# Optimization experiments

Measured on AMD Instinct MI355X. Metric: run time of the kernel, lower is better.

## Reference

```python
import jax, jax.numpy as jnp
import numpy as np

ALPHA = 1.0

def setup_inputs() -> dict:
    key = jax.random.key(0)
    k1, k2, k3, k4 = jax.random.split(key, 4)
    B, N, D = 2048, 32768, 128
    return {
        "anchor": jax.random.normal(k1, (B, D), dtype=jnp.float32),
        "positive": jax.random.normal(k2, (B, D), dtype=jnp.float32),
        "negative": jax.random.normal(k3, (N, D), dtype=jnp.float32),
        "r_score": jax.random.normal(k4, (B, 1), dtype=jnp.float32),
    }

def reference(anchor, positive, negative, r_score):
    # pos_sim: [B,1] elementwise dot per row
    pos_sim = jnp.sum(anchor * positive, axis=1, keepdims=True)
    # neg_mul: [B,N] score matrix; row-wise stable logsumexp -> [B,1]
    neg_mul = jnp.matmul(anchor, negative.T)
    neg_sim = jax.scipy.special.logsumexp(neg_mul, axis=1, keepdims=True)
    loss = jax.nn.relu(neg_sim - pos_sim + r_score + ALPHA)
    return jnp.mean(loss)
```

## Files before the change

kernel.cpp:

```cpp
#include <hip/hip_runtime.h>
#include <hip/hip_bf16.h>


#define B_ROWS 2048
#define N_NEG  32768
#define DIM    128
#define LOG2E  1.4426950408889634f
#define LN2    0.6931471805599453f

typedef __bf16 bf16x8 __attribute__((ext_vector_type(8)));
typedef float  f32x4  __attribute__((ext_vector_type(4)));

static __device__ inline unsigned short f2bf(float f) {
    union { float f; unsigned u; } v; v.f = f;
    unsigned r = v.u + 0x7FFF + ((v.u >> 16) & 1);
    return (unsigned short)(r >> 16);
}

static __device__ inline void load_lds16(const void* g, void* s) {
    __builtin_amdgcn_global_load_lds(
        (const __attribute__((address_space(1))) void*)g,
        (__attribute__((address_space(3))) void*)s,
        16, 0, 0);
}

__global__ void prep(const float* __restrict__ anchor,
                     const float* __restrict__ positive,
                     const float* __restrict__ neg,
                     unsigned short* __restrict__ a_bf,
                     unsigned short* __restrict__ n_bf,
                     float* __restrict__ pos_sim,
                     float* __restrict__ sumexp) {
    int t = threadIdx.x;
    if (blockIdx.x < 256) {
        int row = blockIdx.x * 8 + (t >> 5);
        int c4  = (t & 31) * 4;
        const float4 a4 = *(const float4*)(anchor   + row * DIM + c4);
        const float4 p4 = *(const float4*)(positive + row * DIM + c4);
        float dot = a4.x * p4.x + a4.y * p4.y + a4.z * p4.z + a4.w * p4.w;
        ushort4 ab;
        ab.x = f2bf(a4.x * LOG2E); ab.y = f2bf(a4.y * LOG2E);
        ab.z = f2bf(a4.z * LOG2E); ab.w = f2bf(a4.w * LOG2E);
        *(ushort4*)(a_bf + row * DIM + c4) = ab;
        #pragma unroll
        for (int m = 1; m <= 16; m <<= 1) dot += __shfl_xor(dot, m, 64);
        if ((t & 31) == 0) { pos_sim[row] = dot; sumexp[row] = 0.0f; }
    } else {
        int i = (blockIdx.x - 256) * 256 + t;
        #pragma unroll
        for (int k = 0; k < 4; k++) {
            int idx = i + k * (1024 * 256);
            float4 v = *(const float4*)(neg + (size_t)idx * 4);
            ushort4 o;
            o.x = f2bf(v.x); o.y = f2bf(v.y); o.z = f2bf(v.z); o.w = f2bf(v.w);
            *(ushort4*)(n_bf + (size_t)idx * 4) = o;
        }
    }
}

#define CHUNK 1024
#define TSTEPS (CHUNK / 128)

__global__ __launch_bounds__(256, 2) void fused_gemm_lse(
        const unsigned short* __restrict__ A,
        const unsigned short* __restrict__ Nb,
        float* __restrict__ sumexp) {
    __shared__ unsigned short lds[2][128 * 128];

    const int bid     = blockIdx.x;
    const int rowTile = bid & 15;
    const int chunk   = bid >> 4;
    const int wave = threadIdx.x >> 6, lane = threadIdx.x & 63;
    const int wr = wave >> 1, wc = wave & 1;
    const int q = lane >> 4, c = lane & 15;
    const int lrow = lane >> 4;
    const int lchk = lane & 15;

    const unsigned short* Ag = A + rowTile * (128 * DIM);
    const unsigned short* Bg = Nb + (size_t)(chunk * CHUNK) * DIM;

    #pragma unroll
    for (int i = 0; i < 8; i++) {
        int off = wave * 4096 + i * 512;
        int r   = (off >> 7) + lrow;
        int gofs = r * DIM + ((lchk ^ (r & 7)) << 3);
        load_lds16(Ag + gofs, &lds[0][off]);
        load_lds16(Bg + gofs, &lds[1][off]);
    }
    asm volatile("s_waitcnt vmcnt(0)" ::: "memory");
    __syncthreads();

    int swz[4];
    #pragma unroll
    for (int k = 0; k < 4; k++) swz[k] = (((k * 4 + q) ^ (c & 7)) << 3);

    bf16x8 af[4][4];
    #pragma unroll
    for (int i = 0; i < 4; i++) {
        int row = wr * 64 + i * 16 + c;
        #pragma unroll
        for (int k = 0; k < 4; k++)
            af[i][k] = *(const bf16x8*)&lds[0][row * DIM + swz[k]];
    }
    __syncthreads();

    const f32x4 zero4 = {0.f, 0.f, 0.f, 0.f};
    f32x4 sumacc[4] = {zero4, zero4, zero4, zero4};

    for (int t = 0; t < TSTEPS; t++) {
        const int cur = 1 - (t & 1);
        const int nxt = t & 1;
        if (t + 1 < TSTEPS) {
            const unsigned short* Bn = Bg + (size_t)(t + 1) * 128 * DIM;
            #pragma unroll
            for (int i = 0; i < 8; i++) {
                int off = wave * 4096 + i * 512;
                int r   = (off >> 7) + lrow;
                int gofs = r * DIM + ((lchk ^ (r & 7)) << 3);
                load_lds16(Bn + gofs, &lds[nxt][off]);
            }
        }
        #pragma unroll
        for (int j = 0; j < 4; j++) {
            int brow = wc * 64 + j * 16 + c;
            bf16x8 bf[4];
            #pragma unroll
            for (int k = 0; k < 4; k++)
                bf[k] = *(const bf16x8*)&lds[cur][brow * DIM + swz[k]];
            #pragma unroll
            for (int i = 0; i < 4; i++) {
                f32x4 acc = __builtin_amdgcn_mfma_f32_16x16x32_bf16(af[i][0], bf[0], zero4, 0, 0, 0);
                acc = __builtin_amdgcn_mfma_f32_16x16x32_bf16(af[i][1], bf[1], acc, 0, 0, 0);
                acc = __builtin_amdgcn_mfma_f32_16x16x32_bf16(af[i][2], bf[2], acc, 0, 0, 0);
                acc = __builtin_amdgcn_mfma_f32_16x16x32_bf16(af[i][3], bf[3], acc, 0, 0, 0);
                sumacc[i][0] += __builtin_amdgcn_exp2f(acc[0]);
                sumacc[i][1] += __builtin_amdgcn_exp2f(acc[1]);
                sumacc[i][2] += __builtin_amdgcn_exp2f(acc[2]);
                sumacc[i][3] += __builtin_amdgcn_exp2f(acc[3]);
            }
        }
        if (t + 1 < TSTEPS) {
            asm volatile("s_waitcnt vmcnt(0)" ::: "memory");
            __syncthreads();
        }
    }

    #pragma unroll
    for (int i = 0; i < 4; i++) {
        #pragma unroll
        for (int r = 0; r < 4; r++) {
            float v = sumacc[i][r];
            v += __shfl_xor(v, 1, 64);
            v += __shfl_xor(v, 2, 64);
            v += __shfl_xor(v, 4, 64);
            v += __shfl_xor(v, 8, 64);
            if ((lane & 15) == 0) {
                int row = rowTile * 128 + wr * 64 + i * 16 + q * 4 + r;
                atomicAdd(&sumexp[row], v);
            }
        }
    }
}

__global__ void finalize(const float* __restrict__ sumexp,
                         const float* __restrict__ pos_sim,
                         const float* __restrict__ r_score,
                         float* __restrict__ out) {
    __shared__ float red[4];
    int t = threadIdx.x;
    float acc = 0.0f;
    #pragma unroll
    for (int i = 0; i < 8; i++) {
        int row = t + i * 256;
        float lse  = __log2f(sumexp[row]) * LN2;
        float loss = lse - pos_sim[row] + r_score[row] + 1.0f;
        acc += fmaxf(loss, 0.0f);
    }
    #pragma unroll
    for (int m = 1; m <= 32; m <<= 1) acc += __shfl_xor(acc, m, 64);
    if ((t & 63) == 0) red[t >> 6] = acc;
    __syncthreads();
    if (t == 0) out[0] = (red[0] + red[1] + red[2] + red[3]) * (1.0f / (float)B_ROWS);
}

extern "C" void kernel_launch(void* const* d_in, const int* in_sizes, int n_in,
                              void* d_out, int out_size, void* d_ws, size_t ws_size,
                              hipStream_t stream) {
    const float* anchor   = (const float*)d_in[0];
    const float* positive = (const float*)d_in[1];
    const float* negative = (const float*)d_in[2];
    const float* r_score  = (const float*)d_in[3];
    float* out = (float*)d_out;

    char* ws = (char*)d_ws;
    float* sumexp           = (float*)ws;
    float* pos_sim          = (float*)(ws + 8192);
    unsigned short* a_bf    = (unsigned short*)(ws + 16384);
    unsigned short* n_bf    = (unsigned short*)(ws + 16384 + 524288);

    prep<<<1280, 256, 0, stream>>>(anchor, positive, negative, a_bf, n_bf, pos_sim, sumexp);
    fused_gemm_lse<<<512, 256, 0, stream>>>(a_bf, n_bf, sumexp);
    finalize<<<1, 256, 0, stream>>>(sumexp, pos_sim, r_score, out);
}
```

Before: 95.44 us.

## Keep negatives tile in registers, stream anchors, fuse finalize via last-block counter

The GEMM+logsumexp kernel is restructured so each 512-thread block owns 128 negative rows, holds them in registers as MFMA B operands, and streams all 2048 anchor rows through double-buffered LDS. Each wave loads and reads only its own anchor rows, so the per-step block barrier is gone. Partial sums are staged in LDS and then atomically added per row. The separate finalize kernel is folded in through a completion counter, with the last block computing the mean. The grid drops to 256 blocks and the global atomics per block grow to 2048, which raises contention on the 2048 sumexp addresses.

```diff
diff --git a/kernel.cpp b/kernel.cpp
--- a/kernel.cpp
+++ b/kernel.cpp
@@ -7,6 +7,7 @@
 #define DIM    128
 #define LOG2E  1.4426950408889634f
 #define LN2    0.6931471805599453f
+#define NBLK   256
 
 typedef __bf16 bf16x8 __attribute__((ext_vector_type(8)));
 typedef float  f32x4  __attribute__((ext_vector_type(4)));
@@ -30,9 +31,11 @@
                      unsigned short* __restrict__ a_bf,
                      unsigned short* __restrict__ n_bf,
                      float* __restrict__ pos_sim,
-                     float* __restrict__ sumexp) {
+                     float* __restrict__ sumexp,
+                     int* __restrict__ cnt) {
     int t = threadIdx.x;
     if (blockIdx.x < 256) {
+        if (blockIdx.x == 0 && t == 0) *cnt = 0;
         int row = blockIdx.x * 8 + (t >> 5);
         int c4  = (t & 31) * 4;
         const float4 a4 = *(const float4*)(anchor   + row * DIM + c4);
@@ -58,34 +61,34 @@
     }
 }
 
-#define CHUNK 1024
-#define TSTEPS (CHUNK / 128)
-
-__global__ __launch_bounds__(256, 2) void fused_gemm_lse(
+__global__ __launch_bounds__(512, 2) void fused_gemm_lse(
         const unsigned short* __restrict__ A,
         const unsigned short* __restrict__ Nb,
-        float* __restrict__ sumexp) {
-    __shared__ unsigned short lds[2][128 * 128];
-
-    const int bid     = blockIdx.x;
-    const int rowTile = bid & 15;
-    const int chunk   = bid >> 4;
-    const int wave = threadIdx.x >> 6, lane = threadIdx.x & 63;
-    const int wr = wave >> 1, wc = wave & 1;
+        float* __restrict__ sumexp,
+        const float* __restrict__ pos_sim,
+        const float* __restrict__ r_score,
+        int* __restrict__ cnt,
+        float* __restrict__ out) {
+    __shared__ unsigned short ldsB[128 * 128];
+    __shared__ unsigned short ldsA[2][128 * 128];
+    __shared__ float sumLDS[B_ROWS];
+    __shared__ float red[8];
+    __shared__ int isLast;
+
+    const int tid  = threadIdx.x;
+    const int wave = tid >> 6, lane = tid & 63;
     const int q = lane >> 4, c = lane & 15;
-    const int lrow = lane >> 4;
-    const int lchk = lane & 15;
-
-    const unsigned short* Ag = A + rowTile * (128 * DIM);
-    const unsigned short* Bg = Nb + (size_t)(chunk * CHUNK) * DIM;
-
-    #pragma unroll
-    for (int i = 0; i < 8; i++) {
-        int off = wave * 4096 + i * 512;
+    const int lrow = q, lchk = c;
+    const int bid  = blockIdx.x;
+
+    const unsigned short* Bg = Nb + (size_t)bid * 128 * DIM;
+    #pragma unroll
+    for (int i = 0; i < 4; i++) {
+        int off = wave * 2048 + i * 512;
         int r   = (off >> 7) + lrow;
         int gofs = r * DIM + ((lchk ^ (r & 7)) << 3);
-        load_lds16(Ag + gofs, &lds[0][off]);
-        load_lds16(Bg + gofs, &lds[1][off]);
+        load_lds16(Bg + gofs, &ldsB[off]);
+        load_lds16(A  + gofs, &ldsA[0][off]);
     }
     asm volatile("s_waitcnt vmcnt(0)" ::: "memory");
     __syncthreads();
@@ -94,93 +97,94 @@
     #pragma unroll
     for (int k = 0; k < 4; k++) swz[k] = (((k * 4 + q) ^ (c & 7)) << 3);
 
-    bf16x8 af[4][4];
-    #pragma unroll
-    for (int i = 0; i < 4; i++) {
-        int row = wr * 64 + i * 16 + c;
+    bf16x8 bfr[8][4];
+    #pragma unroll
+    for (int j = 0; j < 8; j++)
         #pragma unroll
         for (int k = 0; k < 4; k++)
-            af[i][k] = *(const bf16x8*)&lds[0][row * DIM + swz[k]];
-    }
-    __syncthreads();
+            bfr[j][k] = *(const bf16x8*)&ldsB[(j * 16 + c) * DIM + swz[k]];
 
     const f32x4 zero4 = {0.f, 0.f, 0.f, 0.f};
-    f32x4 sumacc[4] = {zero4, zero4, zero4, zero4};
-
-    for (int t = 0; t < TSTEPS; t++) {
-        const int cur = 1 - (t & 1);
-        const int nxt = t & 1;
-        if (t + 1 < TSTEPS) {
-            const unsigned short* Bn = Bg + (size_t)(t + 1) * 128 * DIM;
+    const int arow = wave * 16 + c;
+
+    for (int t = 0; t < 16; t++) {
+        const unsigned short* ldsCur = ldsA[t & 1];
+        if (t < 15) {
+            const unsigned short* Ag = A + (size_t)(t + 1) * 128 * DIM;
+            unsigned short* dst = &ldsA[(t + 1) & 1][0];
             #pragma unroll
-            for (int i = 0; i < 8; i++) {
-                int off = wave * 4096 + i * 512;
+            for (int i = 0; i < 4; i++) {
+                int off = wave * 2048 + i * 512;
                 int r   = (off >> 7) + lrow;
                 int gofs = r * DIM + ((lchk ^ (r & 7)) << 3);
-                load_lds16(Bn + gofs, &lds[nxt][off]);
+                load_lds16(Ag + gofs, dst + off);
             }
-        }
-        #pragma unroll
-        for (int j = 0; j < 4; j++) {
-            int brow = wc * 64 + j * 16 + c;
-            bf16x8 bf[4];
-            #pragma unroll
-            for (int k = 0; k < 4; k++)
-                bf[k] = *(const bf16x8*)&lds[cur][brow * DIM + swz[k]];
-            #pragma unroll
-            for (int i = 0; i < 4; i++) {
-                f32x4 acc = __builtin_amdgcn_mfma_f32_16x16x32_bf16(af[i][0], bf[0], zero4, 0, 0, 0);
-                acc = __builtin_amdgcn_mfma_f32_16x16x32_bf16(af[i][1], bf[1], acc, 0, 0, 0);
-                acc = __builtin_amdgcn_mfma_f32_16x16x32_bf16(af[i][2], bf[2], acc, 0, 0, 0);
-                acc = __builtin_amdgcn_mfma_f32_16x16x32_bf16(af[i][3], bf[3], acc, 0, 0, 0);
-                sumacc[i][0] += __builtin_amdgcn_exp2f(acc[0]);
-                sumacc[i][1] += __builtin_amdgcn_exp2f(acc[1]);
-                sumacc[i][2] += __builtin_amdgcn_exp2f(acc[2]);
-                sumacc[i][3] += __builtin_amdgcn_exp2f(acc[3]);
-            }
-        }
-        if (t + 1 < TSTEPS) {
+            asm volatile("s_waitcnt vmcnt(4)" ::: "memory");
+        } else {
             asm volatile("s_waitcnt vmcnt(0)" ::: "memory");
-            __syncthreads();
-        }
-    }
+        }
+
+        bf16x8 af[4];
+        #pragma unroll
+        for (int k = 0; k < 4; k++)
+            af[k] = *(const bf16x8*)&ldsCur[arow * DIM + swz[k]];
+
+        f32x4 sum4 = zero4;
+        #pragma unroll
+        for (int j = 0; j < 8; j++) {
+            f32x4 acc = __builtin_amdgcn_mfma_f32_16x16x32_bf16(af[0], bfr[j][0], zero4, 0, 0, 0);
+            acc = __builtin_amdgcn_mfma_f32_16x16x32_bf16(af[1], bfr[j][1], acc, 0, 0, 0);
+            acc = __builtin_amdgcn_mfma_f32_16x16x32_bf16(af[2], bfr[j][2], acc, 0, 0, 0);
+            acc = __builtin_amdgcn_mfma_f32_16x16x32_bf16(af[3], bfr[j][3], acc, 0, 0, 0);
+            sum4[0] += __builtin_amdgcn_exp2f(acc[0]);
+            sum4[1] += __builtin_amdgcn_exp2f(acc[1]);
+            sum4[2] += __builtin_amdgcn_exp2f(acc[2]);
+            sum4[3] += __builtin_amdgcn_exp2f(acc[3]);
+        }
+        float v0 = sum4[0], v1 = sum4[1], v2 = sum4[2], v3 = sum4[3];
+        #pragma unroll
+        for (int m = 1; m <= 8; m <<= 1) {
+            v0 += __shfl_xor(v0, m, 64);
+            v1 += __shfl_xor(v1, m, 64);
+            v2 += __shfl_xor(v2, m, 64);
+            v3 += __shfl_xor(v3, m, 64);
+        }
+        if ((lane & 15) == 0) {
+            f32x4 w = {v0, v1, v2, v3};
+            *(f32x4*)&sumLDS[t * 128 + wave * 16 + q * 4] = w;
+        }
+    }
+    __syncthreads();
 
     #pragma unroll
     for (int i = 0; i < 4; i++) {
-        #pragma unroll
-        for (int r = 0; r < 4; r++) {
-            float v = sumacc[i][r];
-            v += __shfl_xor(v, 1, 64);
-            v += __shfl_xor(v, 2, 64);
-            v += __shfl_xor(v, 4, 64);
-            v += __shfl_xor(v, 8, 64);
-            if ((lane & 15) == 0) {
-                int row = rowTile * 128 + wr * 64 + i * 16 + q * 4 + r;
-                atomicAdd(&sumexp[row], v);
-            }
-        }
-    }
-}
-
-__global__ void finalize(const float* __restrict__ sumexp,
-                         const float* __restrict__ pos_sim,
-                         const float* __restrict__ r_score,
-                         float* __restrict__ out) {
-    __shared__ float red[4];
-    int t = threadIdx.x;
+        int row = tid + i * 512;
+        atomicAdd(&sumexp[row], sumLDS[row]);
+    }
+    __threadfence();
+    __syncthreads();
+    if (tid == 0) isLast = (atomicAdd(cnt, 1) == NBLK - 1);
+    __syncthreads();
+    if (!isLast) return;
+
     float acc = 0.0f;
     #pragma unroll
-    for (int i = 0; i < 8; i++) {
-        int row = t + i * 256;
-        float lse  = __log2f(sumexp[row]) * LN2;
-        float loss = lse - pos_sim[row] + r_score[row] + 1.0f;
+    for (int i = 0; i < 4; i++) {
+        int row = tid + i * 512;
+        float se   = atomicAdd(&sumexp[row], 0.0f);
+        float loss = __log2f(se) * LN2 - pos_sim[row] + r_score[row] + 1.0f;
         acc += fmaxf(loss, 0.0f);
     }
     #pragma unroll
     for (int m = 1; m <= 32; m <<= 1) acc += __shfl_xor(acc, m, 64);
-    if ((t & 63) == 0) red[t >> 6] = acc;
-    __syncthreads();
-    if (t == 0) out[0] = (red[0] + red[1] + red[2] + red[3]) * (1.0f / (float)B_ROWS);
+    if (lane == 0) red[wave] = acc;
+    __syncthreads();
+    if (tid == 0) {
+        float s = 0.0f;
+        #pragma unroll
+        for (int w = 0; w < 8; w++) s += red[w];
+        out[0] = s * (1.0f / (float)B_ROWS);
+    }
 }
 
 extern "C" void kernel_launch(void* const* d_in, const int* in_sizes, int n_in,
@@ -193,12 +197,14 @@
     float* out = (float*)d_out;
 
     char* ws = (char*)d_ws;
-    float* sumexp           = (float*)ws;
-    float* pos_sim          = (float*)(ws + 8192);
-    unsigned short* a_bf    = (unsigned short*)(ws + 16384);
-    unsigned short* n_bf    = (unsigned short*)(ws + 16384 + 524288);
-
-    prep<<<1280, 256, 0, stream>>>(anchor, positive, negative, a_bf, n_bf, pos_sim, sumexp);
-    fused_gemm_lse<<<512, 256, 0, stream>>>(a_bf, n_bf, sumexp);
-    finalize<<<1, 256, 0, stream>>>(sumexp, pos_sim, r_score, out);
-}
+    float* sumexp        = (float*)ws;
+    float* pos_sim       = (float*)(ws + 8192);
+    int*   cnt           = (int*)(ws + 16384);
+    unsigned short* a_bf = (unsigned short*)(ws + 32768);
+    unsigned short* n_bf = (unsigned short*)(ws + 32768 + 524288);
+
+    prep<<<1280, 256, 0, stream>>>(anchor, positive, negative, a_bf, n_bf,
+                                   pos_sim, sumexp, cnt);
+    fused_gemm_lse<<<NBLK, 512, 0, stream>>>(a_bf, n_bf, sumexp, pos_sim,
+                                             r_score, cnt, out);
+}
```

Result: slower. 127.9 us (+34.0%).
